# Kernel tuning notes

Measured on AMD Instinct MI355X. Metric: run time of the kernel, lower is better.

Reference implementation:

```python
import jax, jax.numpy as jnp
import numpy as np

B, T, D, H = 128, 1024, 256, 256


def setup_inputs() -> dict:
    key = jax.random.key(0)
    ks = jax.random.split(key, 6)
    s_i = 1.0 / np.sqrt(D).astype(np.float32)
    s_h = 1.0 / np.sqrt(H).astype(np.float32)
    obs = jax.random.normal(ks[0], (B, T, D), jnp.float32)
    done = jax.random.randint(ks[1], (B, T), 0, 2).astype(bool)
    init_hstate = jax.random.normal(ks[2], (B, H), jnp.float32)
    # GRU params (flax GRUCell layout): input dense has bias, hidden r/z dense no bias, hidden n dense has bias
    Wi = jax.random.normal(ks[3], (D, 3 * H), jnp.float32) * s_i      # [ir | iz | in]
    bi = jnp.zeros((3 * H,), jnp.float32)
    Wh_rz = jax.random.normal(ks[4], (H, 2 * H), jnp.float32) * s_h   # [hr | hz]
    Wh_n = jax.random.normal(ks[5], (H, H), jnp.float32) * s_h
    bh_n = jnp.zeros((H,), jnp.float32)
    return dict(obs=obs, done=done, init_hstate=init_hstate,
                Wi=Wi, bi=bi, Wh_rz=Wh_rz, Wh_n=Wh_n, bh_n=bh_n)


def reference(obs, done, init_hstate, Wi, bi, Wh_rz, Wh_n, bh_n):
    Hn = Wh_n.shape[0]
    # Precompute all input projections in one big GEMM (same math as per-step dense_i)
    x_proj = obs @ Wi + bi                      # [B, T, 3H]
    x_t = jnp.swapaxes(x_proj, 0, 1)            # [T, B, 3H]
    d_t = jnp.swapaxes(done, 0, 1)              # [T, B]

    def step(h, inp):
        xp, d = inp
        # reset carry to initialize_carry (zeros) where episode is done
        h = jnp.where(d[:, None], 0.0, h)
        hr_hz = h @ Wh_rz                        # [B, 2H]
        r = jax.nn.sigmoid(xp[:, :Hn] + hr_hz[:, :Hn])
        z = jax.nn.sigmoid(xp[:, Hn:2 * Hn] + hr_hz[:, Hn:])
        n = jnp.tanh(xp[:, 2 * Hn:] + r * (h @ Wh_n + bh_n))
        h_new = (1.0 - z) * n + z * h
        return h_new, h_new

    final_h, ys = jax.lax.scan(step, init_hstate, (x_t, d_t))
    return final_h, jnp.swapaxes(ys, 0, 1)      # carry, outputs [B, T, H]
```

## Files before the change

### kernel.cpp

```cpp
#include <hip/hip_runtime.h>
#include <hip/hip_bf16.h>
#include <hip/hip_fp16.h>


#define B_ 128
#define T_ 1024
#define D_ 256
#define H_ 256
#define CHUNKS_ 32
#define CHUNK_T_ (T_ / CHUNKS_)

typedef _Float16 half2v __attribute__((ext_vector_type(2)));
typedef _Float16 half8v __attribute__((ext_vector_type(8)));
typedef float f32x4 __attribute__((ext_vector_type(4)));

__global__ __launch_bounds__(256, 2) void xproj_gemm(
    const float* __restrict__ A,
    const float* __restrict__ W,
    const float* __restrict__ bias,
    _Float16* __restrict__ C)
{
  constexpr int LDS_K = 40;
  __shared__ __align__(16) _Float16 As[128 * LDS_K];
  __shared__ __align__(16) _Float16 Bs[128 * LDS_K];
  const int m0 = blockIdx.x * 128;
  const int n0 = blockIdx.y * 128;
  const int tid = threadIdx.x;
  const int lane = tid & 63;
  const int wv = tid >> 6;
  const int wm = (wv >> 1) * 64;
  const int wn = (wv & 1) * 64;
  const int q = lane >> 4;
  const int lm = lane & 15;

  f32x4 acc[4][4];
#pragma unroll
  for (int i = 0; i < 4; ++i)
#pragma unroll
    for (int j = 0; j < 4; ++j)
      acc[i][j] = (f32x4){0.f, 0.f, 0.f, 0.f};

  const int ar = tid >> 1, ac = (tid & 1) * 16;
  const int bk = tid >> 3, bj = (tid & 7) * 16;

  for (int k0 = 0; k0 < 256; k0 += 32) {
    const float* ap = A + (size_t)(m0 + ar) * 256 + k0 + ac;
    float4 a0 = *(const float4*)(ap + 0);
    float4 a1 = *(const float4*)(ap + 4);
    float4 a2 = *(const float4*)(ap + 8);
    float4 a3 = *(const float4*)(ap + 12);
    const float* bp = W + (size_t)(k0 + bk) * 768 + n0 + bj;
    float4 b0 = *(const float4*)(bp + 0);
    float4 b1 = *(const float4*)(bp + 4);
    float4 b2 = *(const float4*)(bp + 8);
    float4 b3 = *(const float4*)(bp + 12);

    _Float16 av[16];
    av[0] = (_Float16)a0.x; av[1] = (_Float16)a0.y; av[2] = (_Float16)a0.z; av[3] = (_Float16)a0.w;
    av[4] = (_Float16)a1.x; av[5] = (_Float16)a1.y; av[6] = (_Float16)a1.z; av[7] = (_Float16)a1.w;
    av[8] = (_Float16)a2.x; av[9] = (_Float16)a2.y; av[10] = (_Float16)a2.z; av[11] = (_Float16)a2.w;
    av[12] = (_Float16)a3.x; av[13] = (_Float16)a3.y; av[14] = (_Float16)a3.z; av[15] = (_Float16)a3.w;
    *(int4*)&As[ar * LDS_K + ac] = *(int4*)&av[0];
    *(int4*)&As[ar * LDS_K + ac + 8] = *(int4*)&av[8];

    _Float16 bvv[16];
    bvv[0] = (_Float16)b0.x; bvv[1] = (_Float16)b0.y; bvv[2] = (_Float16)b0.z; bvv[3] = (_Float16)b0.w;
    bvv[4] = (_Float16)b1.x; bvv[5] = (_Float16)b1.y; bvv[6] = (_Float16)b1.z; bvv[7] = (_Float16)b1.w;
    bvv[8] = (_Float16)b2.x; bvv[9] = (_Float16)b2.y; bvv[10] = (_Float16)b2.z; bvv[11] = (_Float16)b2.w;
    bvv[12] = (_Float16)b3.x; bvv[13] = (_Float16)b3.y; bvv[14] = (_Float16)b3.z; bvv[15] = (_Float16)b3.w;
#pragma unroll
    for (int i = 0; i < 16; ++i) Bs[(bj + i) * LDS_K + bk] = bvv[i];
    __syncthreads();

    half8v af[4], bfr[4];
#pragma unroll
    for (int i = 0; i < 4; ++i)
      af[i] = *(const half8v*)&As[(wm + i * 16 + lm) * LDS_K + q * 8];
#pragma unroll
    for (int j = 0; j < 4; ++j)
      bfr[j] = *(const half8v*)&Bs[(wn + j * 16 + lm) * LDS_K + q * 8];
#pragma unroll
    for (int i = 0; i < 4; ++i)
#pragma unroll
      for (int j = 0; j < 4; ++j)
        acc[i][j] = __builtin_amdgcn_mfma_f32_16x16x32_f16(af[i], bfr[j], acc[i][j], 0, 0, 0);
    __syncthreads();
  }

#pragma unroll
  for (int j = 0; j < 4; ++j) {
    const int n = n0 + wn + j * 16 + lm;
    const float bv = bias[n];
#pragma unroll
    for (int i = 0; i < 4; ++i) {
#pragma unroll
      for (int r = 0; r < 4; ++r) {
        const int m = m0 + wm + i * 16 + q * 4 + r;
        C[(size_t)m * 768 + n] = (_Float16)(acc[i][j][r] + bv);
      }
    }
  }
}


__device__ __forceinline__ int swzb(int row, int colbyte) {
  return row * 512 + (colbyte ^ ((row & 7) << 4));
}

__global__ __launch_bounds__(256, 1) void gru_scan_mfma(
    const _Float16* __restrict__ xp,
    const int* __restrict__ done,
    const float* __restrict__ h0,
    const float* __restrict__ Wh_rz,
    const float* __restrict__ Wh_n,
    const float* __restrict__ bh_n,
    float* __restrict__ out_final,
    float* __restrict__ out_ys)
{
  const int bx = blockIdx.x;
  const int grp = bx & 7;
  const int chunk = bx >> 3;
  const int t0 = chunk * CHUNK_T_;
  const int tend = t0 + CHUNK_T_;
  const int tid = threadIdx.x;
  const int w = tid >> 6;
  const int l = tid & 63;
  const int lm = l & 15;
  const int q = l >> 4;
  const int colb = w * 64 + lm;

  __shared__ __align__(16) _Float16 h_lds[2][16 * 256];

  half8v bf[3][4][8];
#pragma unroll
  for (int ro = 0; ro < 3; ++ro)
#pragma unroll
    for (int cg = 0; cg < 4; ++cg)
#pragma unroll
      for (int kc = 0; kc < 8; ++kc) {
        half8v v;
#pragma unroll
        for (int j = 0; j < 8; ++j) {
          const int k = kc * 32 + q * 8 + j;
          const int c = colb + cg * 16;
          const float wv = (ro < 2) ? Wh_rz[(size_t)k * 512 + ro * 256 + c]
                                    : Wh_n[(size_t)k * 256 + c];
          v[j] = (_Float16)wv;
        }
        bf[ro][cg][kc] = v;
      }

  float bhn[4];
#pragma unroll
  for (int cg = 0; cg < 4; ++cg) bhn[cg] = bh_n[colb + cg * 16];

  const _Float16* xrow[4];
  float* yrow[4];
  const int* drow[4];
  int dcur[4];
#pragma unroll
  for (int r = 0; r < 4; ++r) {
    const int b = grp * 16 + q * 4 + r;
    xrow[r] = xp + ((size_t)b * T_ + t0) * 768;
    yrow[r] = out_ys + ((size_t)b * T_ + t0) * H_;
    drow[r] = done + (size_t)b * T_ + t0;
    dcur[r] = drow[r][0];
  }

  char* hR = (char*)&h_lds[0][0];
  char* hW = (char*)&h_lds[1][0];
#pragma unroll
  for (int cg = 0; cg < 4; ++cg)
#pragma unroll
    for (int r = 0; r < 4; ++r) {
      const int row = q * 4 + r;
      const int c = colb + cg * 16;
      float v = 0.f;
      if (chunk == 0) {
        const int b = grp * 16 + row;
        v = done[(size_t)b * T_] ? 0.f : h0[(size_t)b * H_ + c];
      }
      *(_Float16*)(hR + swzb(row, c * 2)) = (_Float16)v;
    }
  __syncthreads();

  unsigned act = (chunk == 0) ? 0xFu : 0u;
  unsigned endm = 0u;

  for (int t = t0;;) {
#pragma unroll
    for (int r = 0; r < 4; ++r)
      if (dcur[r]) {
        if (t >= tend) endm |= (1u << r);
        else           act  |= (1u << r);
      }
    if (t >= T_) break;
    if (__all(endm == 0xFu)) break;

    int dn[4];
    const int tn = (t + 1 < T_) ? 1 : 0;
#pragma unroll
    for (int r = 0; r < 4; ++r) {
      const int v = drow[r][tn];
      dn[r] = (t + 1 < T_) ? v : 0;
    }

    half8v a[8];
#pragma unroll
    for (int kc = 0; kc < 8; ++kc)
      a[kc] = *(const half8v*)(hR + swzb(lm, kc * 64 + q * 16));

#pragma unroll
    for (int hf = 0; hf < 2; ++hf) {
      f32x4 acc[3][2];
#pragma unroll
      for (int ro = 0; ro < 3; ++ro)
#pragma unroll
        for (int c2 = 0; c2 < 2; ++c2)
          acc[ro][c2] = (f32x4){0.f, 0.f, 0.f, 0.f};

#pragma unroll
      for (int kc = 0; kc < 8; ++kc)
#pragma unroll
        for (int ro = 0; ro < 3; ++ro)
#pragma unroll
          for (int c2 = 0; c2 < 2; ++c2)
            acc[ro][c2] = __builtin_amdgcn_mfma_f32_16x16x32_f16(
                a[kc], bf[ro][hf * 2 + c2][kc], acc[ro][c2], 0, 0, 0);

#pragma unroll
      for (int c2 = 0; c2 < 2; ++c2) {
        const int cg = hf * 2 + c2;
        const int col = colb + cg * 16;
#pragma unroll
        for (int r = 0; r < 4; ++r) {
          const int row = q * 4 + r;
          const float xr = (float)xrow[r][col];
          const float xz = (float)xrow[r][col + 256];
          const float xn = (float)xrow[r][col + 512];
          const float hm = (float)*(const _Float16*)(hR + swzb(row, col * 2));
          const float sr = xr + acc[0][c2][r];
          const float sz = xz + acc[1][c2][r];
          const float rr = 1.f / (1.f + __expf(-sr));
          const float zz = 1.f / (1.f + __expf(-sz));
          const float npre = xn + rr * (acc[2][c2][r] + bhn[cg]);
          const float e = __expf(-2.f * fabsf(npre));
          const float tv = (1.f - e) / (1.f + e);
          const float nn = npre < 0.f ? -tv : tv;
          const float hnew = (1.f - zz) * nn + zz * hm;
          *(_Float16*)(hW + swzb(row, col * 2)) =
              (_Float16)(dn[r] ? 0.f : hnew);
          if (((act >> r) & 1u) && !((endm >> r) & 1u)) {
            yrow[r][col] = hnew;
            if (t == T_ - 1)
              out_final[(size_t)(grp * 16 + row) * H_ + col] = hnew;
          }
        }
      }
    }

#pragma unroll
    for (int r = 0; r < 4; ++r) {
      xrow[r] += 768;
      yrow[r] += H_;
      drow[r] += 1;
      dcur[r] = dn[r];
    }
    { char* tmp = hR; hR = hW; hW = tmp; }
    ++t;
    __syncthreads();
  }
}

extern "C" void kernel_launch(void* const* d_in, const int* in_sizes, int n_in,
                              void* d_out, int out_size, void* d_ws, size_t ws_size,
                              hipStream_t stream) {
  const float* obs   = (const float*)d_in[0];
  const int*   done  = (const int*)d_in[1];
  const float* h0    = (const float*)d_in[2];
  const float* Wi    = (const float*)d_in[3];
  const float* bi    = (const float*)d_in[4];
  const float* Wh_rz = (const float*)d_in[5];
  const float* Wh_n  = (const float*)d_in[6];
  const float* bh_n  = (const float*)d_in[7];
  float* out = (float*)d_out;
  _Float16* xp = (_Float16*)d_ws;

  xproj_gemm<<<dim3(1024, 6), 256, 0, stream>>>(obs, Wi, bi, xp);
  gru_scan_mfma<<<dim3(256), 256, 0, stream>>>(xp, done, h0, Wh_rz, Wh_n, bh_n,
                                               out, out + B_ * H_);
}
```

Measured before the change: 915.3 us.

## Prefetch next-step xproj tile into LDS asynchronously and fold x into MFMA accumulators

```diff
diff --git a/kernel.cpp b/kernel.cpp
--- a/kernel.cpp
+++ b/kernel.cpp
@@ -105,6 +105,16 @@
 
 __device__ __forceinline__ int swzb(int row, int colbyte) {
   return row * 512 + (colbyte ^ ((row & 7) << 4));
+}
+
+__device__ __forceinline__ int xswz(int row, int colbyte) {
+  return row * 1536 + (colbyte ^ ((row & 7) << 4));
+}
+
+__device__ __forceinline__ void load16_to_lds(const void* g, void* l) {
+  __builtin_amdgcn_global_load_lds(
+      (const __attribute__((address_space(1))) unsigned int*)g,
+      (__attribute__((address_space(3))) unsigned int*)l, 16, 0, 0);
 }
 
 __global__ __launch_bounds__(256, 1) void gru_scan_mfma(
@@ -130,12 +140,13 @@
   const int colb = w * 64 + lm;
 
   __shared__ __align__(16) _Float16 h_lds[2][16 * 256];
+  __shared__ __align__(16) _Float16 xp_lds[2][16 * 768];
 
   half8v bf[3][4][8];
 #pragma unroll
   for (int ro = 0; ro < 3; ++ro)
 #pragma unroll
-    for (int cg = 0; cg < 4; ++cg)
+    for (int cg = 0; cg < 4; ++cg) {
 #pragma unroll
       for (int kc = 0; kc < 8; ++kc) {
         half8v v;
@@ -149,22 +160,32 @@
         }
         bf[ro][cg][kc] = v;
       }
+      __builtin_amdgcn_sched_barrier(0);
+    }
 
   float bhn[4];
 #pragma unroll
   for (int cg = 0; cg < 4; ++cg) bhn[cg] = bh_n[colb + cg * 16];
 
-  const _Float16* xrow[4];
-  float* yrow[4];
-  const int* drow[4];
+  unsigned xsrc[6];
+#pragma unroll
+  for (int j = 0; j < 6; ++j) {
+    const int c = w * 384 + j * 64 + l;
+    const int row = c / 96;
+    const int pc = c - row * 96;
+    const int lc = pc ^ (row & 7);
+    xsrc[j] = (unsigned)((grp * 16 + row) * T_ + t0) * 1536u + (unsigned)lc * 16u;
+  }
+
+  unsigned doff[4];
+  unsigned yoff[4];
   int dcur[4];
 #pragma unroll
   for (int r = 0; r < 4; ++r) {
     const int b = grp * 16 + q * 4 + r;
-    xrow[r] = xp + ((size_t)b * T_ + t0) * 768;
-    yrow[r] = out_ys + ((size_t)b * T_ + t0) * H_;
-    drow[r] = done + (size_t)b * T_ + t0;
-    dcur[r] = drow[r][0];
+    doff[r] = (unsigned)(b * T_ + t0) * 4u;
+    yoff[r] = (unsigned)(b * T_ + t0) * (unsigned)(H_ * 4);
+    dcur[r] = *(const int*)((const char*)done + doff[r]);
   }
 
   char* hR = (char*)&h_lds[0][0];
@@ -182,6 +203,15 @@
       }
       *(_Float16*)(hR + swzb(row, c * 2)) = (_Float16)v;
     }
+
+  {
+    char* xb = (char*)&xp_lds[t0 & 1][0] + w * 6144;
+#pragma unroll
+    for (int j = 0; j < 6; ++j)
+      load16_to_lds((const char*)xp + xsrc[j], xb + j * 1024);
+#pragma unroll
+    for (int j = 0; j < 6; ++j) xsrc[j] += 1536u;
+  }
   __syncthreads();
 
   unsigned act = (chunk == 0) ? 0xFu : 0u;
@@ -197,13 +227,25 @@
     if (t >= T_) break;
     if (__all(endm == 0xFu)) break;
 
+    const bool hasnext = (t + 1 < T_);
+
     int dn[4];
-    const int tn = (t + 1 < T_) ? 1 : 0;
 #pragma unroll
     for (int r = 0; r < 4; ++r) {
-      const int v = drow[r][tn];
-      dn[r] = (t + 1 < T_) ? v : 0;
-    }
+      const int v = *(const int*)((const char*)done + doff[r] + (hasnext ? 4 : 0));
+      dn[r] = hasnext ? v : 0;
+    }
+
+    if (hasnext) {
+      char* xb = (char*)&xp_lds[(t + 1) & 1][0] + w * 6144;
+#pragma unroll
+      for (int j = 0; j < 6; ++j)
+        load16_to_lds((const char*)xp + xsrc[j], xb + j * 1024);
+    }
+#pragma unroll
+    for (int j = 0; j < 6; ++j) xsrc[j] += 1536u;
+
+    const char* xq = (const char*)&xp_lds[t & 1][0];
 
     half8v a[8];
 #pragma unroll
@@ -214,10 +256,16 @@
     for (int hf = 0; hf < 2; ++hf) {
       f32x4 acc[3][2];
 #pragma unroll
-      for (int ro = 0; ro < 3; ++ro)
-#pragma unroll
-        for (int c2 = 0; c2 < 2; ++c2)
-          acc[ro][c2] = (f32x4){0.f, 0.f, 0.f, 0.f};
+      for (int c2 = 0; c2 < 2; ++c2) {
+        const int col = colb + (hf * 2 + c2) * 16;
+#pragma unroll
+        for (int r = 0; r < 4; ++r) {
+          const int row = q * 4 + r;
+          acc[0][c2][r] = (float)*(const _Float16*)(xq + xswz(row, col * 2));
+          acc[1][c2][r] = (float)*(const _Float16*)(xq + xswz(row, (col + 256) * 2));
+          acc[2][c2][r] = bhn[hf * 2 + c2];
+        }
+      }
 
 #pragma unroll
       for (int kc = 0; kc < 8; ++kc)
@@ -230,20 +278,15 @@
 
 #pragma unroll
       for (int c2 = 0; c2 < 2; ++c2) {
-        const int cg = hf * 2 + c2;
-        const int col = colb + cg * 16;
+        const int col = colb + (hf * 2 + c2) * 16;
 #pragma unroll
         for (int r = 0; r < 4; ++r) {
           const int row = q * 4 + r;
-          const float xr = (float)xrow[r][col];
-          const float xz = (float)xrow[r][col + 256];
-          const float xn = (float)xrow[r][col + 512];
+          const float xn = (float)*(const _Float16*)(xq + xswz(row, (col + 512) * 2));
           const float hm = (float)*(const _Float16*)(hR + swzb(row, col * 2));
-          const float sr = xr + acc[0][c2][r];
-          const float sz = xz + acc[1][c2][r];
-          const float rr = 1.f / (1.f + __expf(-sr));
-          const float zz = 1.f / (1.f + __expf(-sz));
-          const float npre = xn + rr * (acc[2][c2][r] + bhn[cg]);
+          const float rr = 1.f / (1.f + __expf(-acc[0][c2][r]));
+          const float zz = 1.f / (1.f + __expf(-acc[1][c2][r]));
+          const float npre = xn + rr * acc[2][c2][r];
           const float e = __expf(-2.f * fabsf(npre));
           const float tv = (1.f - e) / (1.f + e);
           const float nn = npre < 0.f ? -tv : tv;
@@ -251,7 +294,7 @@
           *(_Float16*)(hW + swzb(row, col * 2)) =
               (_Float16)(dn[r] ? 0.f : hnew);
           if (((act >> r) & 1u) && !((endm >> r) & 1u)) {
-            yrow[r][col] = hnew;
+            *(float*)((char*)out_ys + yoff[r] + (unsigned)col * 4u) = hnew;
             if (t == T_ - 1)
               out_final[(size_t)(grp * 16 + row) * H_ + col] = hnew;
           }
@@ -261,9 +304,8 @@
 
 #pragma unroll
     for (int r = 0; r < 4; ++r) {
-      xrow[r] += 768;
-      yrow[r] += H_;
-      drow[r] += 1;
+      doff[r] += 4u;
+      yoff[r] += (unsigned)(H_ * 4);
       dcur[r] = dn[r];
     }
     { char* tmp = hR; hR = hW; hW = tmp; }
```

Measured after the change: 869.4 us. -5.0%, faster.
